# Optimization experiments

Hardware: AMD Instinct MI355X
Metric: run time of the kernel (lower is better)

The kernel has to match this reference:

```python
import jax, jax.numpy as jnp
import numpy as np

B, S, H = 4, 1024, 2560          # batch, seq, hidden_size
E, K, F = 32, 6, 1536            # num_experts, top_k, moe_intermediate_size
SHARED_F = 2 * 1536              # moe_num_shared_experts * moe_intermediate_size
NORM_MIN = 1e-12                 # config.moe_norm_min


def setup_inputs() -> dict:
    key = jax.random.key(0)
    ks = jax.random.split(key, 9)
    rnd = lambda k, shape, scale=0.02: jax.random.normal(k, shape, dtype=jnp.float32) * scale
    return {
        "hidden_states": jax.random.normal(ks[0], (B, S, H), dtype=jnp.float32),
        "router_w": rnd(ks[1], (E, H)),              # Ernie4_5_MoeTopKRouter.weight (fp32)
        "router_bias": jnp.zeros((E,), jnp.float32),  # moe_statics.e_score_correction_bias
        "gate_w": rnd(ks[2], (E, H, F)),
        "up_w": rnd(ks[3], (E, H, F)),
        "down_w": rnd(ks[4], (E, F, H)),
        "shared_gate_w": rnd(ks[5], (H, SHARED_F)),
        "shared_up_w": rnd(ks[6], (H, SHARED_F)),
        "shared_down_w": rnd(ks[7], (SHARED_F, H)),
    }


def _mlp(x, gw, uw, dw):
    # Ernie4_5_MoeMLP: down( silu(gate(x)) * up(x) ), no biases
    return (jax.nn.silu(x @ gw) * (x @ uw)) @ dw


def _forward(hidden_states, router_w, router_bias, gate_w, up_w, down_w,
             shared_gate_w, shared_up_w, shared_down_w):
    T = B * S
    xt = hidden_states.reshape(T, H)

    # shared experts path (always-on dense MLP)
    shared_out = _mlp(xt, shared_gate_w, shared_up_w, shared_down_w)

    # router: fp32 linear -> softmax -> (+ correction bias) -> top-k -> renorm
    logits = xt.astype(jnp.float32) @ router_w.T            # [T, E]
    probs = jax.nn.softmax(logits, axis=-1)
    top_w, top_i = jax.lax.top_k(probs + router_bias[None, :], K)  # [T, K]
    top_w = top_w / jnp.clip(jnp.sum(top_w, axis=-1, keepdims=True), NORM_MIN)
    top_w = top_w.astype(hidden_states.dtype)

    # expert combine: loop over the fixed expert set; per-token combine weight
    # cw[t] = sum_k top_w[t,k] * (top_i[t,k] == e)  (matches one-hot dispatch +
    # index_add_ scatter combine of the original)
    out = jnp.zeros_like(xt)
    for e in range(E):
        cw = jnp.sum(jnp.where(top_i == e, top_w, 0.0), axis=-1)  # [T]
        y = _mlp(xt, gate_w[e], up_w[e], down_w[e])               # [T, H]
        out = out + cw[:, None] * y

    out = out + shared_out
    return out.reshape(B, S, H)


def reference(hidden_states, router_w, router_bias, gate_w, up_w, down_w,
              shared_gate_w, shared_up_w, shared_down_w):
    return _forward(hidden_states, router_w, router_bias, gate_w, up_w, down_w,
                    shared_gate_w, shared_up_w, shared_down_w)
```

## Files before the change

kernel.cpp:

```cpp
#include <hip/hip_runtime.h>
#include <hip/hip_bf16.h>
#include <math.h>

#define T_TOK 4096
#define HID   2560
#define NEXP  32
#define KTOP  6
#define FF    1536
#define SFF   3072
#define MAXP  (T_TOK*KTOP)

typedef __attribute__((ext_vector_type(8))) short short8;
typedef __attribute__((ext_vector_type(4))) float f32x4;

static __device__ __forceinline__ unsigned short f2bf(float x){
  return __builtin_bit_cast(unsigned short, (__bf16)x);
}
static __device__ __forceinline__ float bf2f(unsigned short u){
  unsigned int x = ((unsigned int)u) << 16;
  return __builtin_bit_cast(float, x);
}

static __device__ __forceinline__ void gload_lds16(const void* g, void* l){
  __builtin_amdgcn_global_load_lds(
      (const __attribute__((address_space(1))) unsigned int*)g,
      (__attribute__((address_space(3))) unsigned int*)l, 16, 0, 0);
}

__global__ void k_cast_x(const float* __restrict__ x, unsigned short* __restrict__ xb){
  int i = (blockIdx.x * 256 + threadIdx.x) * 4;
  float4 v = *(const float4*)(x + i);
  ushort4 o;
  o.x = f2bf(v.x); o.y = f2bf(v.y); o.z = f2bf(v.z); o.w = f2bf(v.w);
  *(ushort4*)(xb + i) = o;
}

__global__ __launch_bounds__(256)
void k_transpose(const float* __restrict__ in, unsigned short* __restrict__ out,
                 const int R, const int C, const long long outBS){
  const size_t bi = (size_t)blockIdx.z * (size_t)R * C;
  const size_t bo = (size_t)blockIdx.z * (size_t)outBS;
  __shared__ unsigned short t2[64][72];
  const int r0 = blockIdx.y * 64, c0 = blockIdx.x * 64;
  const int tid = threadIdx.x;
  const int cr = tid & 15;
  const int rr = tid >> 4;
#pragma unroll
  for (int i = 0; i < 4; ++i){
    const int r = rr + 16*i;
    float4 v = *(const float4*)(in + bi + (size_t)(r0 + r)*C + c0 + cr*4);
    ushort4 p;
    p.x = f2bf(v.x); p.y = f2bf(v.y); p.z = f2bf(v.z); p.w = f2bf(v.w);
    *(ushort4*)(&t2[r][cr*4]) = p;
  }
  __syncthreads();
  const int rw = tid & 7;
  const int ro = tid >> 3;
#pragma unroll
  for (int i = 0; i < 2; ++i){
    const int c = ro + 32*i;
    ushort4 a, b;
    a.x = t2[rw*8+0][c]; a.y = t2[rw*8+1][c]; a.z = t2[rw*8+2][c]; a.w = t2[rw*8+3][c];
    b.x = t2[rw*8+4][c]; b.y = t2[rw*8+5][c]; b.z = t2[rw*8+6][c]; b.w = t2[rw*8+7][c];
    unsigned short* op = out + bo + (size_t)(c0 + c)*R + r0 + rw*8;
    *(ushort4*)(op)     = a;
    *(ushort4*)(op + 4) = b;
  }
}

__global__ void k_router(const float* __restrict__ x, const float* __restrict__ rw,
                         const float* __restrict__ rb, float* __restrict__ top_w,
                         int* __restrict__ top_i, int* __restrict__ counts){
  const int lane = threadIdx.x & 63;
  const int wv   = threadIdx.x >> 6;
  const int t    = blockIdx.x * 4 + wv;
  const float* xr = x + (size_t)t * HID;
  float xv[40];
#pragma unroll
  for (int i = 0; i < 40; ++i) xv[i] = xr[lane + 64*i];
  float sc[32];
  for (int e = 0; e < 32; ++e){
    const float* w = rw + (size_t)e * HID;
    float s = 0.f;
#pragma unroll
    for (int i = 0; i < 40; ++i) s = fmaf(xv[i], w[lane + 64*i], s);
#pragma unroll
    for (int o = 32; o; o >>= 1) s += __shfl_xor(s, o);
    sc[e] = s;
  }
  float mx = sc[0];
#pragma unroll
  for (int e = 1; e < 32; ++e) mx = fmaxf(mx, sc[e]);
  float se = 0.f;
#pragma unroll
  for (int e = 0; e < 32; ++e){ sc[e] = expf(sc[e] - mx); se += sc[e]; }
  const float inv = 1.f / se;
#pragma unroll
  for (int e = 0; e < 32; ++e) sc[e] = sc[e] * inv + rb[e];

  unsigned chosen = 0; float swv[KTOP]; int sid[KTOP]; float wsum = 0.f;
#pragma unroll
  for (int k = 0; k < KTOP; ++k){
    float bv = -1e30f; int bi = 0;
#pragma unroll
    for (int e = 0; e < 32; ++e){
      bool ok = !((chosen >> e) & 1u);
      if (ok && sc[e] > bv){ bv = sc[e]; bi = e; }
    }
    chosen |= 1u << bi; swv[k] = bv; sid[k] = bi; wsum += bv;
  }
  const float dn = fmaxf(wsum, 1e-12f);
  if (lane < KTOP){
    top_w[t*KTOP + lane] = swv[lane] / dn;
    top_i[t*KTOP + lane] = sid[lane];
    atomicAdd(counts + sid[lane], 1);
  }
}

__global__ void k_scan(const int* __restrict__ counts, int* __restrict__ offsets){
  if (threadIdx.x == 0){
    int a = 0;
    for (int e = 0; e < NEXP; ++e){ offsets[e] = a; a += counts[e]; }
    offsets[NEXP] = a;
  }
}

__global__ void k_scatter(const int* __restrict__ top_i, const float* __restrict__ top_w,
                          const int* __restrict__ offsets, int* __restrict__ cursor,
                          int* __restrict__ pair_tok, float* __restrict__ pair_w){
  const int t = blockIdx.x * 256 + threadIdx.x;
  if (t >= T_TOK) return;
#pragma unroll
  for (int k = 0; k < KTOP; ++k){
    int e = top_i[t*KTOP + k];
    int pos = offsets[e] + atomicAdd(cursor + e, 1);
    pair_tok[pos] = t;
    pair_w[pos]   = top_w[t*KTOP + k];
  }
}

template<int F8>
__global__ __launch_bounds__(256)
void k_swiglu(const unsigned short* __restrict__ y, unsigned short* __restrict__ act){
  const int i = blockIdx.x * 256 + threadIdx.x;
  const int p = i / F8, c = i % F8;
  const unsigned short* row = y + (size_t)p * (2*F8*8);
  short8 g8 = *(const short8*)(row + c*8);
  short8 u8 = *(const short8*)(row + F8*8 + c*8);
  short8 o;
#pragma unroll
  for (int j = 0; j < 8; ++j){
    float g = bf2f((unsigned short)g8[j]);
    float u = bf2f((unsigned short)u8[j]);
    float s = (g / (1.f + expf(-g))) * u;
    o[j] = (short)f2bf(s);
  }
  *(short8*)(act + (size_t)p*F8*8 + c*8) = o;
}

template<bool GROUPED, bool GATHER, int OUT>
__global__ __launch_bounds__(512, 2)
void k_gemm(const unsigned short* __restrict__ A,
            const unsigned short* __restrict__ BT,
            void* __restrict__ outp,
            const int* __restrict__ pair_tok, const float* __restrict__ pair_w,
            const int* __restrict__ counts, const int* __restrict__ offsets,
            const int N, const int K, const int ntiles)
{
  const int NH = K >> 5;
  const int total = gridDim.x;
  const int phys  = blockIdx.x;
  const int logical = (phys & 7) * (total >> 3) + (phys >> 3);
  const int mt   = logical & 15;
  const int rest = logical >> 4;
  const int n0 = (rest % ntiles) << 8;
  const int e  = rest / ntiles;

  int M, base;
  if (GROUPED){ M = counts[e]; base = offsets[e]; }
  else        { M = T_TOK;     base = 0; }
  if (mt * 256 >= M) return;
  const unsigned short* Bb = BT + (size_t)e * (size_t)N * K;

  __shared__ unsigned short AS[4*8192];
  __shared__ unsigned short BS[4*8192];

  const int tid  = threadIdx.x;
  const int lane = tid & 63;
  const int w    = tid >> 6;
  const int wr = w >> 2, wc = w & 3;

  const int lrow = lane >> 2, lchunk = lane & 3;
  const int swz = (lchunk ^ ((lrow >> 1) & 3)) * 8;
  const unsigned short *ap0, *ap1, *bp0, *bp1;
  {
    const int r0 = w*32 + lrow, r1 = w*32 + 16 + lrow;
    int i0 = min(mt*256 + r0, M - 1);
    int i1 = min(mt*256 + r1, M - 1);
    int rowA0 = GATHER ? pair_tok[base + i0] : (GROUPED ? base + i0 : i0);
    int rowA1 = GATHER ? pair_tok[base + i1] : (GROUPED ? base + i1 : i1);
    ap0 = A + (size_t)rowA0 * K + swz;
    ap1 = A + (size_t)rowA1 * K + swz;
    bp0 = Bb + (size_t)(n0 + r0) * K + swz;
    bp1 = Bb + (size_t)(n0 + r1) * K + swz;
  }

  const f32x4 zero = {0.f,0.f,0.f,0.f};
  f32x4 acc[8][4];
#pragma unroll
  for (int m = 0; m < 8; ++m)
#pragma unroll
    for (int n = 0; n < 4; ++n) acc[m][n] = zero;

  const int fr = lane & 15;
  const int fg = ((lane >> 4) ^ ((lane >> 1) & 3)) * 16;

#define STAGE(h)                                                            \
  { const int _s = (h) & 3; const size_t _k = (size_t)(h) * 32;             \
    gload_lds16(ap0 + _k, (char*)AS + _s*16384 + (w*32)*64);                \
    gload_lds16(ap1 + _k, (char*)AS + _s*16384 + (w*32+16)*64);             \
    gload_lds16(bp0 + _k, (char*)BS + _s*16384 + (w*32)*64);                \
    gload_lds16(bp1 + _k, (char*)BS + _s*16384 + (w*32+16)*64); }

  STAGE(0) STAGE(1) STAGE(2)
  asm volatile("s_waitcnt vmcnt(8)" ::: "memory");
  __builtin_amdgcn_s_barrier();

#pragma unroll 4
  for (int h = 0; h < NH; ++h){
    const int s = h & 3;
    const char* _as = (const char*)AS + s*16384;
    const char* _bs = (const char*)BS + s*16384;
    short8 bq[4], af[8];
#pragma unroll
    for (int n = 0; n < 4; ++n)
      bq[n] = *(const short8*)(_bs + (wc*64 + n*16 + fr)*64 + fg);
#pragma unroll
    for (int m = 0; m < 8; ++m)
      af[m] = *(const short8*)(_as + (wr*128 + m*16 + fr)*64 + fg);
    if (h + 3 < NH) STAGE(h + 3)
    __builtin_amdgcn_s_setprio(1);
#pragma unroll
    for (int m = 0; m < 8; ++m)
#pragma unroll
      for (int n = 0; n < 4; ++n)
        acc[m][n] = __builtin_amdgcn_mfma_f32_16x16x32_bf16(af[m], bq[n], acc[m][n], 0, 0, 0);
    __builtin_amdgcn_s_setprio(0);
    if (h + 3 < NH)      asm volatile("s_waitcnt vmcnt(8)" ::: "memory");
    else if (h + 2 < NH) asm volatile("s_waitcnt vmcnt(4)" ::: "memory");
    else if (h + 1 < NH) asm volatile("s_waitcnt vmcnt(0)" ::: "memory");
    __builtin_amdgcn_s_barrier();
  }
#undef STAGE

#pragma unroll
  for (int m = 0; m < 8; ++m)
#pragma unroll
    for (int j = 0; j < 4; ++j){
      const int rr = mt*256 + wr*128 + m*16 + (lane >> 4)*4 + j;
      if (rr < M){
        const int col = n0 + wc*64 + (lane & 15);
        if (OUT == 0){
          unsigned short* orow = (unsigned short*)outp + (size_t)(base + rr) * N + col;
#pragma unroll
          for (int n = 0; n < 4; ++n) orow[n*16] = f2bf(acc[m][n][j]);
        } else if (OUT == 1){
          const int p = base + rr;
          const int tok = pair_tok[p];
          const float pw = pair_w[p];
          float* orow = (float*)outp + (size_t)tok * HID + col;
#pragma unroll
          for (int n = 0; n < 4; ++n) atomicAdd(orow + n*16, acc[m][n][j] * pw);
        } else {
          float* orow = (float*)outp + (size_t)rr * N + col;
#pragma unroll
          for (int n = 0; n < 4; ++n) orow[n*16] = acc[m][n][j];
        }
      }
    }
}

extern "C" void kernel_launch(void* const* d_in, const int* in_sizes, int n_in,
                              void* d_out, int out_size, void* d_ws, size_t ws_size,
                              hipStream_t stream)
{
  (void)in_sizes; (void)n_in; (void)out_size; (void)ws_size;
  const float* hid = (const float*)d_in[0];
  const float* rw  = (const float*)d_in[1];
  const float* rb  = (const float*)d_in[2];
  const float* gw  = (const float*)d_in[3];
  const float* uw  = (const float*)d_in[4];
  const float* dw  = (const float*)d_in[5];
  const float* sgw = (const float*)d_in[6];
  const float* suw = (const float*)d_in[7];
  const float* sdw = (const float*)d_in[8];
  float* out = (float*)d_out;

  char* ws = (char*)d_ws;
  size_t o = 0;
  unsigned short* xb   = (unsigned short*)(ws + o); o += (size_t)T_TOK*HID*2;
  unsigned short* act  = (unsigned short*)(ws + o); o += (size_t)MAXP*FF*2;
  unsigned short* sact = (unsigned short*)(ws + o); o += (size_t)T_TOK*SFF*2;
  unsigned short* y    = (unsigned short*)(ws + o); o += (size_t)MAXP*2*FF*2;
  unsigned short* sy   = (unsigned short*)(ws + o); o += (size_t)T_TOK*2*SFF*2;
  unsigned short* Wbuf = (unsigned short*)(ws + o);
  unsigned short* guT  = Wbuf;
  unsigned short* sguT = Wbuf + (size_t)NEXP*2*FF*HID;
  unsigned short* dT   = Wbuf;
  unsigned short* sdT  = Wbuf + (size_t)NEXP*HID*FF;
  o += (size_t)NEXP*2*FF*HID*2 + (size_t)2*SFF*HID*2;
  float* top_w    = (float*)(ws + o); o += (size_t)T_TOK*KTOP*4;
  int*   top_i    = (int*)(ws + o);   o += (size_t)T_TOK*KTOP*4;
  float* pair_w   = (float*)(ws + o); o += (size_t)MAXP*4;
  int*   pair_tok = (int*)(ws + o);   o += (size_t)MAXP*4;
  int*   counts   = (int*)(ws + o);   o += NEXP*4;
  int*   offsets  = (int*)(ws + o);   o += (NEXP+1)*4;
  int*   cursor   = (int*)(ws + o);   o += NEXP*4;

  hipMemsetAsync(counts, 0, (NEXP + (NEXP+1) + NEXP) * sizeof(int), stream);

  k_cast_x<<<(T_TOK*HID)/1024, 256, 0, stream>>>(hid, xb);
  k_router<<<T_TOK/4, 256, 0, stream>>>(hid, rw, rb, top_w, top_i, counts);
  k_scan<<<1, 64, 0, stream>>>(counts, offsets);
  k_scatter<<<T_TOK/256, 256, 0, stream>>>(top_i, top_w, offsets, cursor, pair_tok, pair_w);

  k_transpose<<<dim3(FF/64,  HID/64, NEXP), 256, 0, stream>>>(gw,  guT,                    HID, FF,  (long long)2*FF*HID);
  k_transpose<<<dim3(FF/64,  HID/64, NEXP), 256, 0, stream>>>(uw,  guT + (size_t)FF*HID,   HID, FF,  (long long)2*FF*HID);
  k_transpose<<<dim3(SFF/64, HID/64, 1),    256, 0, stream>>>(sgw, sguT,                   HID, SFF, 0);
  k_transpose<<<dim3(SFF/64, HID/64, 1),    256, 0, stream>>>(suw, sguT + (size_t)SFF*HID, HID, SFF, 0);

  k_gemm<true,  true,  0><<<16*(2*FF/256)*NEXP, 512, 0, stream>>>(
      xb, guT, y, pair_tok, nullptr, counts, offsets, 2*FF, HID, 2*FF/256);
  k_gemm<false, false, 0><<<16*(2*SFF/256), 512, 0, stream>>>(
      xb, sguT, sy, nullptr, nullptr, nullptr, nullptr, 2*SFF, HID, 2*SFF/256);
  k_swiglu<FF/8><<<(MAXP*(FF/8))/256, 256, 0, stream>>>(y, act);
  k_swiglu<SFF/8><<<(T_TOK*(SFF/8))/256, 256, 0, stream>>>(sy, sact);

  k_transpose<<<dim3(HID/64, FF/64,  NEXP), 256, 0, stream>>>(dw,  dT,  FF,  HID, (long long)HID*FF);
  k_transpose<<<dim3(HID/64, SFF/64, 1),    256, 0, stream>>>(sdw, sdT, SFF, HID, 0);

  k_gemm<false, false, 2><<<16*(HID/256), 512, 0, stream>>>(
      sact, sdT, out, nullptr, nullptr, nullptr, nullptr, HID, SFF, HID/256);
  k_gemm<true,  false, 1><<<16*(HID/256)*NEXP, 512, 0, stream>>>(
      act, dT, out, pair_tok, pair_w, counts, offsets, HID, FF, HID/256);
}
```

Baseline: 1.792 ms.

## Fuse fp32 weight transpose and bf16 cast into GEMM B-tile loading

Measured after the change: 3.968 ms. 121% more time.

```diff
diff --git a/kernel.cpp b/kernel.cpp
--- a/kernel.cpp
+++ b/kernel.cpp
@@ -20,6 +20,9 @@
   unsigned int x = ((unsigned int)u) << 16;
   return __builtin_bit_cast(float, x);
 }
+static __device__ __forceinline__ unsigned int pk2bf(float a, float b){
+  return (unsigned int)f2bf(a) | ((unsigned int)f2bf(b) << 16);
+}
 
 static __device__ __forceinline__ void gload_lds16(const void* g, void* l){
   __builtin_amdgcn_global_load_lds(
@@ -33,39 +36,6 @@
   ushort4 o;
   o.x = f2bf(v.x); o.y = f2bf(v.y); o.z = f2bf(v.z); o.w = f2bf(v.w);
   *(ushort4*)(xb + i) = o;
-}
-
-__global__ __launch_bounds__(256)
-void k_transpose(const float* __restrict__ in, unsigned short* __restrict__ out,
-                 const int R, const int C, const long long outBS){
-  const size_t bi = (size_t)blockIdx.z * (size_t)R * C;
-  const size_t bo = (size_t)blockIdx.z * (size_t)outBS;
-  __shared__ unsigned short t2[64][72];
-  const int r0 = blockIdx.y * 64, c0 = blockIdx.x * 64;
-  const int tid = threadIdx.x;
-  const int cr = tid & 15;
-  const int rr = tid >> 4;
-#pragma unroll
-  for (int i = 0; i < 4; ++i){
-    const int r = rr + 16*i;
-    float4 v = *(const float4*)(in + bi + (size_t)(r0 + r)*C + c0 + cr*4);
-    ushort4 p;
-    p.x = f2bf(v.x); p.y = f2bf(v.y); p.z = f2bf(v.z); p.w = f2bf(v.w);
-    *(ushort4*)(&t2[r][cr*4]) = p;
-  }
-  __syncthreads();
-  const int rw = tid & 7;
-  const int ro = tid >> 3;
-#pragma unroll
-  for (int i = 0; i < 2; ++i){
-    const int c = ro + 32*i;
-    ushort4 a, b;
-    a.x = t2[rw*8+0][c]; a.y = t2[rw*8+1][c]; a.z = t2[rw*8+2][c]; a.w = t2[rw*8+3][c];
-    b.x = t2[rw*8+4][c]; b.y = t2[rw*8+5][c]; b.z = t2[rw*8+6][c]; b.w = t2[rw*8+7][c];
-    unsigned short* op = out + bo + (size_t)(c0 + c)*R + r0 + rw*8;
-    *(ushort4*)(op)     = a;
-    *(ushort4*)(op + 4) = b;
-  }
 }
 
 __global__ void k_router(const float* __restrict__ x, const float* __restrict__ rw,
@@ -158,14 +128,14 @@
   *(short8*)(act + (size_t)p*F8*8 + c*8) = o;
 }
 
-template<bool GROUPED, bool GATHER, int OUT>
-__global__ __launch_bounds__(512, 2)
+template<bool GROUPED, bool GATHER, int OUT, bool HASB2>
+__global__ __launch_bounds__(512, 1)
 void k_gemm(const unsigned short* __restrict__ A,
-            const unsigned short* __restrict__ BT,
+            const float* __restrict__ Bg, const float* __restrict__ Bu,
             void* __restrict__ outp,
             const int* __restrict__ pair_tok, const float* __restrict__ pair_w,
             const int* __restrict__ counts, const int* __restrict__ offsets,
-            const int N, const int K, const int ntiles)
+            const int N, const int K, const int strideB, const int ntiles)
 {
   const int NH = K >> 5;
   const int total = gridDim.x;
@@ -173,14 +143,23 @@
   const int logical = (phys & 7) * (total >> 3) + (phys >> 3);
   const int mt   = logical & 15;
   const int rest = logical >> 4;
-  const int n0 = (rest % ntiles) << 8;
-  const int e  = rest / ntiles;
+  const int nt   = rest % ntiles;
+  const int e    = rest / ntiles;
+  const int n0   = nt << 8;
 
   int M, base;
   if (GROUPED){ M = counts[e]; base = offsets[e]; }
   else        { M = T_TOK;     base = 0; }
   if (mt * 256 >= M) return;
-  const unsigned short* Bb = BT + (size_t)e * (size_t)N * K;
+
+  const float* bsrcbase;
+  int ncol0;
+  if (HASB2){
+    const int split = ntiles >> 1;
+    if (nt < split){ bsrcbase = Bg; ncol0 = nt << 8; }
+    else           { bsrcbase = Bu; ncol0 = (nt - split) << 8; }
+  } else { bsrcbase = Bg; ncol0 = nt << 8; }
+  if (GROUPED) bsrcbase += (size_t)e * (size_t)K * strideB;
 
   __shared__ unsigned short AS[4*8192];
   __shared__ unsigned short BS[4*8192];
@@ -191,19 +170,24 @@
   const int wr = w >> 2, wc = w & 3;
 
   const int lrow = lane >> 2, lchunk = lane & 3;
-  const int swz = (lchunk ^ ((lrow >> 1) & 3)) * 8;
-  const unsigned short *ap0, *ap1, *bp0, *bp1;
+  const unsigned short *ap0, *ap1;
   {
     const int r0 = w*32 + lrow, r1 = w*32 + 16 + lrow;
+    const int swz = (lchunk ^ ((r0 >> 1) & 3)) * 8;
     int i0 = min(mt*256 + r0, M - 1);
     int i1 = min(mt*256 + r1, M - 1);
     int rowA0 = GATHER ? pair_tok[base + i0] : (GROUPED ? base + i0 : i0);
     int rowA1 = GATHER ? pair_tok[base + i1] : (GROUPED ? base + i1 : i1);
     ap0 = A + (size_t)rowA0 * K + swz;
     ap1 = A + (size_t)rowA1 * K + swz;
-    bp0 = Bb + (size_t)(n0 + r0) * K + swz;
-    bp1 = Bb + (size_t)(n0 + r1) * K + swz;
-  }
+  }
+
+  const int kg = w & 3;
+  const int nh = w >> 2;
+  const int nn0 = nh*128 + 2*lane;
+  const float* bsrc = bsrcbase + (size_t)(kg*8) * strideB + ncol0 + nn0;
+  const int wslot = (kg ^ ((nn0 >> 1) & 3)) * 16;
+  const int wbyte0 = nn0*64 + wslot;
 
   const f32x4 zero = {0.f,0.f,0.f,0.f};
   f32x4 acc[8][4];
@@ -215,15 +199,36 @@
   const int fr = lane & 15;
   const int fg = ((lane >> 4) ^ ((lane >> 1) & 3)) * 16;
 
-#define STAGE(h)                                                            \
+  float2 breg[2][8];
+
+#define LOADB(buf, h)                                                       \
+  { const float* _b = bsrc + (size_t)(h) * 32 * strideB;                    \
+    _Pragma("unroll")                                                       \
+    for (int j = 0; j < 8; ++j) breg[buf][j] = *(const float2*)(_b + (size_t)j * strideB); }
+
+#define CVTWRITE(buf, sl)                                                   \
+  { uint4 u0, u1;                                                           \
+    u0.x = pk2bf(breg[buf][0].x, breg[buf][1].x);                           \
+    u0.y = pk2bf(breg[buf][2].x, breg[buf][3].x);                           \
+    u0.z = pk2bf(breg[buf][4].x, breg[buf][5].x);                           \
+    u0.w = pk2bf(breg[buf][6].x, breg[buf][7].x);                           \
+    u1.x = pk2bf(breg[buf][0].y, breg[buf][1].y);                           \
+    u1.y = pk2bf(breg[buf][2].y, breg[buf][3].y);                           \
+    u1.z = pk2bf(breg[buf][4].y, breg[buf][5].y);                           \
+    u1.w = pk2bf(breg[buf][6].y, breg[buf][7].y);                           \
+    *(uint4*)((char*)BS + (sl)*16384 + wbyte0)      = u0;                   \
+    *(uint4*)((char*)BS + (sl)*16384 + wbyte0 + 64) = u1; }
+
+#define STAGEA(h)                                                           \
   { const int _s = (h) & 3; const size_t _k = (size_t)(h) * 32;             \
     gload_lds16(ap0 + _k, (char*)AS + _s*16384 + (w*32)*64);                \
-    gload_lds16(ap1 + _k, (char*)AS + _s*16384 + (w*32+16)*64);             \
-    gload_lds16(bp0 + _k, (char*)BS + _s*16384 + (w*32)*64);                \
-    gload_lds16(bp1 + _k, (char*)BS + _s*16384 + (w*32+16)*64); }
-
-  STAGE(0) STAGE(1) STAGE(2)
-  asm volatile("s_waitcnt vmcnt(8)" ::: "memory");
+    gload_lds16(ap1 + _k, (char*)AS + _s*16384 + (w*32+16)*64); }
+
+  LOADB(0, 0)
+  STAGEA(0) STAGEA(1) STAGEA(2)
+  CVTWRITE(0, 0)
+  LOADB(1, 1)
+  asm volatile("s_waitcnt vmcnt(0) lgkmcnt(0)" ::: "memory");
   __builtin_amdgcn_s_barrier();
 
 #pragma unroll 4
@@ -238,7 +243,9 @@
 #pragma unroll
     for (int m = 0; m < 8; ++m)
       af[m] = *(const short8*)(_as + (wr*128 + m*16 + fr)*64 + fg);
-    if (h + 3 < NH) STAGE(h + 3)
+    if (h + 2 < NH) LOADB(h & 1, h + 2)
+    if (h + 3 < NH) STAGEA(h + 3)
+    if (h + 1 < NH) CVTWRITE((h + 1) & 1, (h + 1) & 3)
     __builtin_amdgcn_s_setprio(1);
 #pragma unroll
     for (int m = 0; m < 8; ++m)
@@ -246,12 +253,16 @@
       for (int n = 0; n < 4; ++n)
         acc[m][n] = __builtin_amdgcn_mfma_f32_16x16x32_bf16(af[m], bq[n], acc[m][n], 0, 0, 0);
     __builtin_amdgcn_s_setprio(0);
-    if (h + 3 < NH)      asm volatile("s_waitcnt vmcnt(8)" ::: "memory");
-    else if (h + 2 < NH) asm volatile("s_waitcnt vmcnt(4)" ::: "memory");
-    else if (h + 1 < NH) asm volatile("s_waitcnt vmcnt(0)" ::: "memory");
-    __builtin_amdgcn_s_barrier();
-  }
-#undef STAGE
+    if (h + 1 < NH){
+      if (h + 3 < NH)      asm volatile("s_waitcnt vmcnt(10) lgkmcnt(0)" ::: "memory");
+      else if (h + 2 < NH) asm volatile("s_waitcnt vmcnt(8) lgkmcnt(0)" ::: "memory");
+      else                 asm volatile("s_waitcnt vmcnt(0) lgkmcnt(0)" ::: "memory");
+      __builtin_amdgcn_s_barrier();
+    }
+  }
+#undef LOADB
+#undef CVTWRITE
+#undef STAGEA
 
 #pragma unroll
   for (int m = 0; m < 8; ++m)
@@ -259,7 +270,7 @@
     for (int j = 0; j < 4; ++j){
       const int rr = mt*256 + wr*128 + m*16 + (lane >> 4)*4 + j;
       if (rr < M){
-        const int col = n0 + wc*64 + (lane & 15);
+        const int col = n0 + wc*64 + fr;
         if (OUT == 0){
           unsigned short* orow = (unsigned short*)outp + (size_t)(base + rr) * N + col;
 #pragma unroll
@@ -303,12 +314,6 @@
   unsigned short* sact = (unsigned short*)(ws + o); o += (size_t)T_TOK*SFF*2;
   unsigned short* y    = (unsigned short*)(ws + o); o += (size_t)MAXP*2*FF*2;
   unsigned short* sy   = (unsigned short*)(ws + o); o += (size_t)T_TOK*2*SFF*2;
-  unsigned short* Wbuf = (unsigned short*)(ws + o);
-  unsigned short* guT  = Wbuf;
-  unsigned short* sguT = Wbuf + (size_t)NEXP*2*FF*HID;
-  unsigned short* dT   = Wbuf;
-  unsigned short* sdT  = Wbuf + (size_t)NEXP*HID*FF;
-  o += (size_t)NEXP*2*FF*HID*2 + (size_t)2*SFF*HID*2;
   float* top_w    = (float*)(ws + o); o += (size_t)T_TOK*KTOP*4;
   int*   top_i    = (int*)(ws + o);   o += (size_t)T_TOK*KTOP*4;
   float* pair_w   = (float*)(ws + o); o += (size_t)MAXP*4;
@@ -324,23 +329,15 @@
   k_scan<<<1, 64, 0, stream>>>(counts, offsets);
   k_scatter<<<T_TOK/256, 256, 0, stream>>>(top_i, top_w, offsets, cursor, pair_tok, pair_w);
 
-  k_transpose<<<dim3(FF/64,  HID/64, NEXP), 256, 0, stream>>>(gw,  guT,                    HID, FF,  (long long)2*FF*HID);
-  k_transpose<<<dim3(FF/64,  HID/64, NEXP), 256, 0, stream>>>(uw,  guT + (size_t)FF*HID,   HID, FF,  (long long)2*FF*HID);
-  k_transpose<<<dim3(SFF/64, HID/64, 1),    256, 0, stream>>>(sgw, sguT,                   HID, SFF, 0);
-  k_transpose<<<dim3(SFF/64, HID/64, 1),    256, 0, stream>>>(suw, sguT + (size_t)SFF*HID, HID, SFF, 0);
-
-  k_gemm<true,  true,  0><<<16*(2*FF/256)*NEXP, 512, 0, stream>>>(
-      xb, guT, y, pair_tok, nullptr, counts, offsets, 2*FF, HID, 2*FF/256);
-  k_gemm<false, false, 0><<<16*(2*SFF/256), 512, 0, stream>>>(
-      xb, sguT, sy, nullptr, nullptr, nullptr, nullptr, 2*SFF, HID, 2*SFF/256);
+  k_gemm<true,  true,  0, true><<<16*(2*FF/256)*NEXP, 512, 0, stream>>>(
+      xb, gw, uw, y, pair_tok, nullptr, counts, offsets, 2*FF, HID, FF, 2*FF/256);
+  k_gemm<false, false, 0, true><<<16*(2*SFF/256), 512, 0, stream>>>(
+      xb, sgw, suw, sy, nullptr, nullptr, nullptr, nullptr, 2*SFF, HID, SFF, 2*SFF/256);
   k_swiglu<FF/8><<<(MAXP*(FF/8))/256, 256, 0, stream>>>(y, act);
   k_swiglu<SFF/8><<<(T_TOK*(SFF/8))/256, 256, 0, stream>>>(sy, sact);
 
-  k_transpose<<<dim3(HID/64, FF/64,  NEXP), 256, 0, stream>>>(dw,  dT,  FF,  HID, (long long)HID*FF);
-  k_transpose<<<dim3(HID/64, SFF/64, 1),    256, 0, stream>>>(sdw, sdT, SFF, HID, 0);
-
-  k_gemm<false, false, 2><<<16*(HID/256), 512, 0, stream>>>(
-      sact, sdT, out, nullptr, nullptr, nullptr, nullptr, HID, SFF, HID/256);
-  k_gemm<true,  false, 1><<<16*(HID/256)*NEXP, 512, 0, stream>>>(
-      act, dT, out, pair_tok, pair_w, counts, offsets, HID, FF, HID/256);
-}
+  k_gemm<false, false, 2, false><<<16*(HID/256), 512, 0, stream>>>(
+      sact, sdw, nullptr, out, nullptr, nullptr, nullptr, nullptr, HID, SFF, HID, HID/256);
+  k_gemm<true,  false, 1, false><<<16*(HID/256)*NEXP, 512, 0, stream>>>(
+      act, dw, nullptr, out, pair_tok, pair_w, counts, offsets, HID, FF, HID, HID/256);
+}
```
